# Performance work log

Measured on AMD Instinct MI355X. Metric: run time of the kernel, lower is better.

Reference implementation:

```python
import jax, jax.numpy as jnp
import numpy as np

N = 50000
E = 800000
IN_DIM = 256
HID = 256
EMB = 64


def _glorot(key, shape):
    fan_in, fan_out = shape[0], shape[1]
    lim = jnp.sqrt(6.0 / (fan_in + fan_out)).astype(jnp.float32)
    return jax.random.uniform(key, shape, jnp.float32, -lim, lim)


def sage_conv(x, src, dst, W_neigh, W_root, b, num_nodes):
    # PyG SAGEConv (aggr='mean', root_weight=True):
    #   out = mean_{j in N(i)} x_j @ W_neigh + x_i @ W_root + b
    msgs = x[src]                                              # [E, F] gather
    s = jax.ops.segment_sum(msgs, dst, num_segments=num_nodes)  # [N, F]
    cnt = jax.ops.segment_sum(jnp.ones((msgs.shape[0],), x.dtype), dst,
                              num_segments=num_nodes)           # [N]
    mean = s / jnp.maximum(cnt, 1.0)[:, None]
    return mean @ W_neigh + x @ W_root + b


def encode(x, src, dst, W1n, W1r, b1, W2n, W2r, b2):
    h = sage_conv(x, src, dst, W1n, W1r, b1, x.shape[0])
    h = jax.nn.relu(h)  # dropout omitted (eval mode)
    return sage_conv(h, src, dst, W2n, W2r, b2, x.shape[0])


def setup_inputs() -> dict:
    key = jax.random.key(0)
    ks = jax.random.split(key, 20)
    inp = {
        "user_x": jax.random.normal(ks[0], (N, IN_DIM), jnp.float32),
        "item_x": jax.random.normal(ks[1], (N, IN_DIM), jnp.float32),
        "user_edge_index": jax.random.randint(ks[2], (2, E), 0, N),
        "item_edge_index": jax.random.randint(ks[3], (2, E), 0, N),
        # user encoder params
        "u1_Wn": _glorot(ks[4], (IN_DIM, HID)), "u1_Wr": _glorot(ks[5], (IN_DIM, HID)),
        "u1_b": jnp.zeros((HID,), jnp.float32),
        "u2_Wn": _glorot(ks[6], (HID, EMB)), "u2_Wr": _glorot(ks[7], (HID, EMB)),
        "u2_b": jnp.zeros((EMB,), jnp.float32),
        # item encoder params
        "i1_Wn": _glorot(ks[8], (IN_DIM, HID)), "i1_Wr": _glorot(ks[9], (IN_DIM, HID)),
        "i1_b": jnp.zeros((HID,), jnp.float32),
        "i2_Wn": _glorot(ks[10], (HID, EMB)), "i2_Wr": _glorot(ks[11], (HID, EMB)),
        "i2_b": jnp.zeros((EMB,), jnp.float32),
        # scoring head: Linear(2*EMB, 1)
        "head_W": _glorot(ks[12], (2 * EMB, 1)),
        "head_b": jnp.zeros((1,), jnp.float32),
    }
    return inp


def reference(user_x, item_x, user_edge_index, item_edge_index,
              u1_Wn, u1_Wr, u1_b, u2_Wn, u2_Wr, u2_b,
              i1_Wn, i1_Wr, i1_b, i2_Wn, i2_Wr, i2_b,
              head_W, head_b):
    u_src, u_dst = user_edge_index[0], user_edge_index[1]
    i_src, i_dst = item_edge_index[0], item_edge_index[1]
    user_emb = encode(user_x, u_src, u_dst, u1_Wn, u1_Wr, u1_b, u2_Wn, u2_Wr, u2_b)
    item_emb = encode(item_x, i_src, i_dst, i1_Wn, i1_Wr, i1_b, i2_Wn, i2_Wr, i2_b)
    combined = jnp.concatenate([user_emb, item_emb], axis=-1)   # [N, 2*EMB]
    return jax.nn.sigmoid(combined @ head_W + head_b)           # [N, 1]
```

## Files before the change

### kernel.cpp

```cpp
#include <hip/hip_runtime.h>
#include <cstdint>
#include <cstddef>

#define N_NODES 50000
#define N_EDGES 800000
#define IN_DIM 256
#define HID 256
#define EMB 64
#define SCAN_B 1024
#define NBLK ((N_NODES + SCAN_B - 1) / SCAN_B)

typedef __attribute__((ext_vector_type(8))) short bf16x8v;
typedef __attribute__((ext_vector_type(4))) float f32x4v;

__device__ inline ushort f2bf(float f) {
    uint32_t u = __float_as_uint(f);
    uint32_t r = (u + 0x7FFFu + ((u >> 16) & 1u)) >> 16;
    return (ushort)r;
}
__device__ inline float bf2f(ushort b) {
    return __uint_as_float((uint32_t)b << 16);
}

__global__ void hist_kernel(const int* __restrict__ dst, int* __restrict__ cnt, int E) {
    int e = blockIdx.x * blockDim.x + threadIdx.x;
    if (e < E) atomicAdd(&cnt[dst[e]], 1);
}

__global__ void scan_local(const int* __restrict__ cnt, int* __restrict__ loc,
                           int* __restrict__ bsum, int n) {
    __shared__ int buf[SCAN_B];
    int tid = threadIdx.x;
    int i = blockIdx.x * SCAN_B + tid;
    int v = (i < n) ? cnt[i] : 0;
    buf[tid] = v;
    __syncthreads();
    #pragma unroll
    for (int off = 1; off < SCAN_B; off <<= 1) {
        int t = (tid >= off) ? buf[tid - off] : 0;
        __syncthreads();
        buf[tid] += t;
        __syncthreads();
    }
    if (i < n) loc[i] = buf[tid] - v;
    if (tid == SCAN_B - 1) bsum[blockIdx.x] = buf[SCAN_B - 1];
}

__global__ void scan_bsum(int* __restrict__ bsum, int nb, int* __restrict__ total_out) {
    __shared__ int b[64];
    int tid = threadIdx.x;
    int v = (tid < nb) ? bsum[tid] : 0;
    b[tid] = v;
    __syncthreads();
    #pragma unroll
    for (int off = 1; off < 64; off <<= 1) {
        int t = (tid >= off) ? b[tid - off] : 0;
        __syncthreads();
        b[tid] += t;
        __syncthreads();
    }
    if (tid < nb) bsum[tid] = b[tid] - v;
    if (tid == 63) *total_out = b[63];
}

__global__ void scan_add(int* __restrict__ loc_cursor, const int* __restrict__ bsum,
                         int* __restrict__ offs, int n) {
    int i = blockIdx.x * SCAN_B + threadIdx.x;
    if (i < n) {
        int o = loc_cursor[i] + bsum[blockIdx.x];
        offs[i] = o;
        loc_cursor[i] = o;
    }
}

__global__ void fill_kernel(const int* __restrict__ src, const int* __restrict__ dst,
                            int* __restrict__ cursor, int* __restrict__ ssrc, int E) {
    int e = blockIdx.x * blockDim.x + threadIdx.x;
    if (e < E) {
        int d = dst[e];
        int pos = atomicAdd(&cursor[d], 1);
        ssrc[pos] = src[e];
    }
}

__global__ void cvt_split(const float* __restrict__ x, ushort* __restrict__ xh,
                          ushort* __restrict__ xl, int n4) {
    int i = blockIdx.x * blockDim.x + threadIdx.x;
    if (i >= n4) return;
    float4 v = ((const float4*)x)[i];
    ushort4 h, l;
    h.x = f2bf(v.x); l.x = f2bf(v.x - bf2f(h.x));
    h.y = f2bf(v.y); l.y = f2bf(v.y - bf2f(h.y));
    h.z = f2bf(v.z); l.z = f2bf(v.z - bf2f(h.z));
    h.w = f2bf(v.w); l.w = f2bf(v.w - bf2f(h.w));
    ((ushort4*)xh)[i] = h;
    ((ushort4*)xl)[i] = l;
}

__global__ void cvt_wT(const float* __restrict__ B1, const float* __restrict__ B2,
                       ushort* __restrict__ th, ushort* __restrict__ tl, int Nhalf) {
    int idx = blockIdx.x * blockDim.x + threadIdx.x;
    if (idx >= 2 * Nhalf * 256) return;
    int nn = idx >> 8;
    int k  = idx & 255;
    const float* Bp = (nn < Nhalf) ? B1 : B2;
    int col = (nn < Nhalf) ? nn : nn - Nhalf;
    float v = Bp[(size_t)k * Nhalf + col];
    ushort h = f2bf(v);
    th[idx] = h;
    tl[idx] = f2bf(v - bf2f(h));
}

__global__ __launch_bounds__(256) void gemm_bf16x3(
        const ushort* __restrict__ Ah, const ushort* __restrict__ Al,
        const ushort* __restrict__ BTh, const ushort* __restrict__ BTl,
        ushort* __restrict__ Cb, float* __restrict__ Cf,
        int M, int nsplit, int ldf) {
    __shared__ ushort As[2][128 * 32];

    int tid  = threadIdx.x;
    int lane = tid & 63;
    int wv   = tid >> 6;
    int wm   = wv >> 1;
    int wn   = wv & 1;
    int rowBase = blockIdx.x * 128;
    int colBase = blockIdx.y * 128;

    int sr = tid & 127;
    int sm = tid >> 7;
    const ushort* Ag = sm ? Al : Ah;
    int grow = rowBase + sr;
    bool rok = grow < M;
    int sxor = (sr >> 1) & 3;

    int fr = lane & 15;
    int fc = lane >> 4;
    int axor = (fr >> 1) & 3;

    f32x4v zero4 = {0.f, 0.f, 0.f, 0.f};
    f32x4v acc[4][4];
    #pragma unroll
    for (int a = 0; a < 4; ++a)
        #pragma unroll
        for (int b = 0; b < 4; ++b) acc[a][b] = zero4;

    for (int k0 = 0; k0 < 256; k0 += 32) {
        __syncthreads();
        {
            const ushort* gs = Ag + (size_t)grow * 256 + k0;
            #pragma unroll
            for (int s = 0; s < 4; ++s) {
                uint4 v = rok ? *(const uint4*)(gs + s * 8) : make_uint4(0u, 0u, 0u, 0u);
                *(uint4*)&As[sm][sr * 32 + (s ^ sxor) * 8] = v;
            }
        }
        __syncthreads();

        bf16x8v afh[4], afl[4];
        #pragma unroll
        for (int mf = 0; mf < 4; ++mf) {
            int row = wm * 64 + mf * 16 + fr;
            int addr = row * 32 + ((fc ^ axor) * 8);
            afh[mf] = *(const bf16x8v*)&As[0][addr];
            afl[mf] = *(const bf16x8v*)&As[1][addr];
        }
        #pragma unroll
        for (int nf = 0; nf < 4; ++nf) {
            int col = colBase + wn * 64 + nf * 16 + fr;
            size_t boff = (size_t)col * 256 + k0 + fc * 8;
            bf16x8v bfh = *(const bf16x8v*)(BTh + boff);
            bf16x8v bfl = *(const bf16x8v*)(BTl + boff);
            #pragma unroll
            for (int mf = 0; mf < 4; ++mf) {
                acc[mf][nf] = __builtin_amdgcn_mfma_f32_16x16x32_bf16(
                                  afh[mf], bfh, acc[mf][nf], 0, 0, 0);
                acc[mf][nf] = __builtin_amdgcn_mfma_f32_16x16x32_bf16(
                                  afh[mf], bfl, acc[mf][nf], 0, 0, 0);
                acc[mf][nf] = __builtin_amdgcn_mfma_f32_16x16x32_bf16(
                                  afl[mf], bfh, acc[mf][nf], 0, 0, 0);
            }
        }
    }

    #pragma unroll
    for (int mf = 0; mf < 4; ++mf) {
        #pragma unroll
        for (int nf = 0; nf < 4; ++nf) {
            int col = colBase + wn * 64 + nf * 16 + fr;
            #pragma unroll
            for (int r = 0; r < 4; ++r) {
                int row = rowBase + wm * 64 + mf * 16 + fc * 4 + r;
                if (row < M) {
                    float v = acc[mf][nf][r];
                    if (col < nsplit)
                        Cb[(size_t)row * nsplit + col] = f2bf(v);
                    else
                        Cf[(size_t)row * ldf + (col - nsplit)] = v;
                }
            }
        }
    }
}

__global__ void combine1_kernel(const ushort* __restrict__ t1b,
                                const float* __restrict__ r1,
                                const int* __restrict__ offs,
                                const int* __restrict__ ssrc,
                                const float* __restrict__ b1,
                                ushort* __restrict__ hh, ushort* __restrict__ hl,
                                int n) {
    int gtid = blockIdx.x * blockDim.x + threadIdx.x;
    int node = gtid >> 6;
    int lane = gtid & 63;
    if (node >= n) return;
    int beg = offs[node];
    int end = offs[node + 1];
    const ushort4* t = (const ushort4*)t1b;
    float4 s = make_float4(0.f, 0.f, 0.f, 0.f);
    int e = beg;
    for (; e + 1 < end; e += 2) {
        int s0 = ssrc[e];
        int s1 = ssrc[e + 1];
        ushort4 q0 = t[(size_t)s0 * 64 + lane];
        ushort4 q1 = t[(size_t)s1 * 64 + lane];
        s.x += bf2f(q0.x) + bf2f(q1.x);
        s.y += bf2f(q0.y) + bf2f(q1.y);
        s.z += bf2f(q0.z) + bf2f(q1.z);
        s.w += bf2f(q0.w) + bf2f(q1.w);
    }
    if (e < end) {
        ushort4 q0 = t[(size_t)ssrc[e] * 64 + lane];
        s.x += bf2f(q0.x); s.y += bf2f(q0.y);
        s.z += bf2f(q0.z); s.w += bf2f(q0.w);
    }
    int deg = end - beg;
    float inv = 1.0f / (float)(deg > 0 ? deg : 1);
    float4 r = ((const float4*)r1)[(size_t)node * 64 + lane];
    float4 bb = ((const float4*)b1)[lane];
    float o0 = s.x * inv + r.x + bb.x;
    float o1 = s.y * inv + r.y + bb.y;
    float o2 = s.z * inv + r.z + bb.z;
    float o3 = s.w * inv + r.w + bb.w;
    o0 = o0 > 0.f ? o0 : 0.f;
    o1 = o1 > 0.f ? o1 : 0.f;
    o2 = o2 > 0.f ? o2 : 0.f;
    o3 = o3 > 0.f ? o3 : 0.f;
    ushort4 h, l;
    h.x = f2bf(o0); l.x = f2bf(o0 - bf2f(h.x));
    h.y = f2bf(o1); l.y = f2bf(o1 - bf2f(h.y));
    h.z = f2bf(o2); l.z = f2bf(o2 - bf2f(h.z));
    h.w = f2bf(o3); l.w = f2bf(o3 - bf2f(h.w));
    ((ushort4*)hh)[(size_t)node * 64 + lane] = h;
    ((ushort4*)hl)[(size_t)node * 64 + lane] = l;
}

__global__ void combine2_kernel(const ushort* __restrict__ t2b,
                                const float* __restrict__ r2,
                                const int* __restrict__ offs,
                                const int* __restrict__ ssrc,
                                const float* __restrict__ b2,
                                float* __restrict__ emb, int n) {
    int gtid = blockIdx.x * blockDim.x + threadIdx.x;
    int node = gtid >> 6;
    int lane = gtid & 63;
    if (node >= n) return;
    int beg = offs[node];
    int end = offs[node + 1];
    float s = 0.f;
    int e = beg;
    for (; e + 1 < end; e += 2) {
        int s0 = ssrc[e];
        int s1 = ssrc[e + 1];
        float v0 = bf2f(t2b[(size_t)s0 * 64 + lane]);
        float v1 = bf2f(t2b[(size_t)s1 * 64 + lane]);
        s += v0 + v1;
    }
    if (e < end) s += bf2f(t2b[(size_t)ssrc[e] * 64 + lane]);
    int deg = end - beg;
    float inv = 1.0f / (float)(deg > 0 ? deg : 1);
    emb[(size_t)node * 64 + lane] =
        s * inv + r2[(size_t)node * 64 + lane] + b2[lane];
}

__global__ void head_kernel(const float* __restrict__ eu, const float* __restrict__ ei,
                            const float* __restrict__ hW, const float* __restrict__ hb,
                            float* __restrict__ out, int n) {
    __shared__ float w[128];
    __shared__ float b0;
    if (threadIdx.x < 128) w[threadIdx.x] = hW[threadIdx.x];
    if (threadIdx.x == 0) b0 = hb[0];
    __syncthreads();
    int i = blockIdx.x * blockDim.x + threadIdx.x;
    if (i >= n) return;
    const float4* a = (const float4*)(eu + (size_t)i * 64);
    const float4* c = (const float4*)(ei + (size_t)i * 64);
    float s = b0;
    #pragma unroll
    for (int j = 0; j < 16; ++j) {
        float4 v = a[j];
        s += v.x * w[j * 4 + 0] + v.y * w[j * 4 + 1] + v.z * w[j * 4 + 2] + v.w * w[j * 4 + 3];
    }
    #pragma unroll
    for (int j = 0; j < 16; ++j) {
        float4 v = c[j];
        s += v.x * w[64 + j * 4 + 0] + v.y * w[64 + j * 4 + 1] + v.z * w[64 + j * 4 + 2] + v.w * w[64 + j * 4 + 3];
    }
    out[i] = 1.0f / (1.0f + __expf(-s));
}

extern "C" void kernel_launch(void* const* d_in, const int* in_sizes, int n_in,
                              void* d_out, int out_size, void* d_ws, size_t ws_size,
                              hipStream_t stream) {
    const float* user_x = (const float*)d_in[0];
    const float* item_x = (const float*)d_in[1];
    const int*   u_ei   = (const int*)d_in[2];
    const int*   i_ei   = (const int*)d_in[3];
    const float* u1_Wn = (const float*)d_in[4];
    const float* u1_Wr = (const float*)d_in[5];
    const float* u1_b  = (const float*)d_in[6];
    const float* u2_Wn = (const float*)d_in[7];
    const float* u2_Wr = (const float*)d_in[8];
    const float* u2_b  = (const float*)d_in[9];
    const float* i1_Wn = (const float*)d_in[10];
    const float* i1_Wr = (const float*)d_in[11];
    const float* i1_b  = (const float*)d_in[12];
    const float* i2_Wn = (const float*)d_in[13];
    const float* i2_Wr = (const float*)d_in[14];
    const float* i2_b  = (const float*)d_in[15];
    const float* head_W = (const float*)d_in[16];
    const float* head_b = (const float*)d_in[17];
    float* out = (float*)d_out;

    char* p = (char*)d_ws;
    auto alloc = [&](size_t bytes) -> void* {
        void* r = (void*)p;
        p += (bytes + 255) & ~(size_t)255;
        return r;
    };
    int* cnt_u  = (int*)alloc((size_t)N_NODES * 4);
    int* cnt_i  = (int*)alloc((size_t)N_NODES * 4);
    int* offs_u = (int*)alloc((size_t)(N_NODES + 1) * 4);
    int* offs_i = (int*)alloc((size_t)(N_NODES + 1) * 4);
    int* cur_u  = (int*)alloc((size_t)N_NODES * 4);
    int* cur_i  = (int*)alloc((size_t)N_NODES * 4);
    int* bsum_u = (int*)alloc((size_t)64 * 4);
    int* bsum_i = (int*)alloc((size_t)64 * 4);
    int* ssrc_u = (int*)alloc((size_t)N_EDGES * 4);
    int* ssrc_i = (int*)alloc((size_t)N_EDGES * 4);
    ushort* xh  = (ushort*)alloc((size_t)N_NODES * 256 * 2);
    ushort* xl  = (ushort*)alloc((size_t)N_NODES * 256 * 2);
    ushort* hh  = (ushort*)alloc((size_t)N_NODES * 256 * 2);
    ushort* hl  = (ushort*)alloc((size_t)N_NODES * 256 * 2);
    ushort* w1h = (ushort*)alloc((size_t)512 * 256 * 2);
    ushort* w1l = (ushort*)alloc((size_t)512 * 256 * 2);
    ushort* w2h = (ushort*)alloc((size_t)128 * 256 * 2);
    ushort* w2l = (ushort*)alloc((size_t)128 * 256 * 2);
    ushort* t1b = (ushort*)alloc((size_t)N_NODES * 256 * 2);
    float*  r1  = (float*)alloc((size_t)N_NODES * 256 * 4);
    ushort* t2b = (ushort*)alloc((size_t)N_NODES * 64 * 2);
    float*  r2  = (float*)alloc((size_t)N_NODES * 64 * 4);
    float* emb_u = (float*)alloc((size_t)N_NODES * EMB * 4);
    float* emb_i = (float*)alloc((size_t)N_NODES * EMB * 4);

    hipMemsetAsync(cnt_u, 0, (size_t)N_NODES * 4, stream);
    hipMemsetAsync(cnt_i, 0, (size_t)N_NODES * 4, stream);

    const int* u_src = u_ei;
    const int* u_dst = u_ei + N_EDGES;
    const int* i_src = i_ei;
    const int* i_dst = i_ei + N_EDGES;

    int egrid = (N_EDGES + 255) / 256;
    int sgrid = (N_NODES * 64 + 255) / 256;
    int mgrid128 = (N_NODES + 127) / 128;
    int cvt_x_grid = (N_NODES * 256 / 4 + 255) / 256;

    hist_kernel<<<egrid, 256, 0, stream>>>(u_dst, cnt_u, N_EDGES);
    hist_kernel<<<egrid, 256, 0, stream>>>(i_dst, cnt_i, N_EDGES);
    scan_local<<<NBLK, SCAN_B, 0, stream>>>(cnt_u, cur_u, bsum_u, N_NODES);
    scan_local<<<NBLK, SCAN_B, 0, stream>>>(cnt_i, cur_i, bsum_i, N_NODES);
    scan_bsum<<<1, 64, 0, stream>>>(bsum_u, NBLK, offs_u + N_NODES);
    scan_bsum<<<1, 64, 0, stream>>>(bsum_i, NBLK, offs_i + N_NODES);
    scan_add<<<NBLK, SCAN_B, 0, stream>>>(cur_u, bsum_u, offs_u, N_NODES);
    scan_add<<<NBLK, SCAN_B, 0, stream>>>(cur_i, bsum_i, offs_i, N_NODES);
    fill_kernel<<<egrid, 256, 0, stream>>>(u_src, u_dst, cur_u, ssrc_u, N_EDGES);
    fill_kernel<<<egrid, 256, 0, stream>>>(i_src, i_dst, cur_i, ssrc_i, N_EDGES);

    cvt_split<<<cvt_x_grid, 256, 0, stream>>>(user_x, xh, xl, N_NODES * 256 / 4);
    cvt_wT<<<(2 * 256 * 256 + 255) / 256, 256, 0, stream>>>(u1_Wn, u1_Wr, w1h, w1l, 256);
    cvt_wT<<<(2 * 64 * 256 + 255) / 256, 256, 0, stream>>>(u2_Wn, u2_Wr, w2h, w2l, 64);
    {
        dim3 g(mgrid128, 4);
        gemm_bf16x3<<<g, 256, 0, stream>>>(xh, xl, w1h, w1l, t1b, r1, N_NODES, 256, 256);
    }
    combine1_kernel<<<sgrid, 256, 0, stream>>>(t1b, r1, offs_u, ssrc_u, u1_b, hh, hl, N_NODES);
    {
        dim3 g(mgrid128, 1);
        gemm_bf16x3<<<g, 256, 0, stream>>>(hh, hl, w2h, w2l, t2b, r2, N_NODES, 64, 64);
    }
    combine2_kernel<<<sgrid, 256, 0, stream>>>(t2b, r2, offs_u, ssrc_u, u2_b, emb_u, N_NODES);

    cvt_split<<<cvt_x_grid, 256, 0, stream>>>(item_x, xh, xl, N_NODES * 256 / 4);
    cvt_wT<<<(2 * 256 * 256 + 255) / 256, 256, 0, stream>>>(i1_Wn, i1_Wr, w1h, w1l, 256);
    cvt_wT<<<(2 * 64 * 256 + 255) / 256, 256, 0, stream>>>(i2_Wn, i2_Wr, w2h, w2l, 64);
    {
        dim3 g(mgrid128, 4);
        gemm_bf16x3<<<g, 256, 0, stream>>>(xh, xl, w1h, w1l, t1b, r1, N_NODES, 256, 256);
    }
    combine1_kernel<<<sgrid, 256, 0, stream>>>(t1b, r1, offs_i, ssrc_i, i1_b, hh, hl, N_NODES);
    {
        dim3 g(mgrid128, 1);
        gemm_bf16x3<<<g, 256, 0, stream>>>(hh, hl, w2h, w2l, t2b, r2, N_NODES, 64, 64);
    }
    combine2_kernel<<<sgrid, 256, 0, stream>>>(t2b, r2, offs_i, ssrc_i, i2_b, emb_i, N_NODES);

    head_kernel<<<(N_NODES + 255) / 256, 256, 0, stream>>>(emb_u, emb_i, head_W,
                                                           head_b, out, N_NODES);
}
```

Baseline: 892.6 us.

## Stage full-K A row panel in LDS once and loop over column groups

The GEMM now loads a 64-row by 256-K panel of both hi and lo A operands into shared memory once per block, then iterates over column groups of 128 inside the block. Previously each block reloaded A per 128-column tile, with a K-loop and two barriers per step. This cuts redundant A reads from global memory and removes the per-K synchronisation. The cost is 64KB of LDS per block, which lowers occupancy, and each block now does up to four column groups serially.

```diff
diff --git a/kernel.cpp b/kernel.cpp
--- a/kernel.cpp
+++ b/kernel.cpp
@@ -9,6 +9,7 @@
 #define EMB 64
 #define SCAN_B 1024
 #define NBLK ((N_NODES + SCAN_B - 1) / SCAN_B)
+#define BR 64
 
 typedef __attribute__((ext_vector_type(8))) short bf16x8v;
 typedef __attribute__((ext_vector_type(4))) float f32x4v;
@@ -111,91 +112,90 @@
     tl[idx] = f2bf(v - bf2f(h));
 }
 
-__global__ __launch_bounds__(256) void gemm_bf16x3(
+__global__ __launch_bounds__(256) void gemm_bf16x3_v2(
         const ushort* __restrict__ Ah, const ushort* __restrict__ Al,
         const ushort* __restrict__ BTh, const ushort* __restrict__ BTl,
         ushort* __restrict__ Cb, float* __restrict__ Cf,
-        int M, int nsplit, int ldf) {
-    __shared__ ushort As[2][128 * 32];
+        int M, int nsplit, int ldf, int ncg) {
+    __shared__ ushort As[2][BR * 256];
 
     int tid  = threadIdx.x;
     int lane = tid & 63;
     int wv   = tid >> 6;
     int wm   = wv >> 1;
     int wn   = wv & 1;
-    int rowBase = blockIdx.x * 128;
-    int colBase = blockIdx.y * 128;
-
-    int sr = tid & 127;
-    int sm = tid >> 7;
-    const ushort* Ag = sm ? Al : Ah;
-    int grow = rowBase + sr;
-    bool rok = grow < M;
-    int sxor = (sr >> 1) & 3;
+    int rowBase = blockIdx.x * BR;
+
+    #pragma unroll
+    for (int i = 0; i < 16; ++i) {
+        int gidx = i * 256 + tid;
+        int sm   = gidx >> 11;
+        int rem  = gidx & 2047;
+        int row  = rem >> 5;
+        int slot = rem & 31;
+        const ushort* Ag = sm ? Al : Ah;
+        int gr = rowBase + row;
+        uint4 v = (gr < M) ? *(const uint4*)(Ag + (size_t)gr * 256 + slot * 8)
+                           : make_uint4(0u, 0u, 0u, 0u);
+        *(uint4*)&As[sm][row * 256 + ((slot ^ (row & 7)) * 8)] = v;
+    }
+    __syncthreads();
 
     int fr = lane & 15;
     int fc = lane >> 4;
-    int axor = (fr >> 1) & 3;
-
-    f32x4v zero4 = {0.f, 0.f, 0.f, 0.f};
-    f32x4v acc[4][4];
-    #pragma unroll
-    for (int a = 0; a < 4; ++a)
+
+    for (int cg = 0; cg < ncg; ++cg) {
+        f32x4v zero4 = {0.f, 0.f, 0.f, 0.f};
+        f32x4v acc[2][4];
         #pragma unroll
-        for (int b = 0; b < 4; ++b) acc[a][b] = zero4;
-
-    for (int k0 = 0; k0 < 256; k0 += 32) {
-        __syncthreads();
-        {
-            const ushort* gs = Ag + (size_t)grow * 256 + k0;
+        for (int a = 0; a < 2; ++a)
             #pragma unroll
-            for (int s = 0; s < 4; ++s) {
-                uint4 v = rok ? *(const uint4*)(gs + s * 8) : make_uint4(0u, 0u, 0u, 0u);
-                *(uint4*)&As[sm][sr * 32 + (s ^ sxor) * 8] = v;
+            for (int b = 0; b < 4; ++b) acc[a][b] = zero4;
+
+        #pragma unroll
+        for (int k0 = 0; k0 < 8; ++k0) {
+            bf16x8v afh[2], afl[2];
+            #pragma unroll
+            for (int mf = 0; mf < 2; ++mf) {
+                int row   = wm * 32 + mf * 16 + fr;
+                int kslot = (k0 * 4 + fc) ^ (row & 7);
+                int addr  = row * 256 + kslot * 8;
+                afh[mf] = *(const bf16x8v*)&As[0][addr];
+                afl[mf] = *(const bf16x8v*)&As[1][addr];
+            }
+            #pragma unroll
+            for (int nf = 0; nf < 4; ++nf) {
+                int col = cg * 128 + wn * 64 + nf * 16 + fr;
+                size_t boff = (size_t)col * 256 + k0 * 32 + fc * 8;
+                bf16x8v bfh = *(const bf16x8v*)(BTh + boff);
+                bf16x8v bfl = *(const bf16x8v*)(BTl + boff);
+                #pragma unroll
+                for (int mf = 0; mf < 2; ++mf) {
+                    acc[mf][nf] = __builtin_amdgcn_mfma_f32_16x16x32_bf16(
+                                      afh[mf], bfh, acc[mf][nf], 0, 0, 0);
+                    acc[mf][nf] = __builtin_amdgcn_mfma_f32_16x16x32_bf16(
+                                      afh[mf], bfl, acc[mf][nf], 0, 0, 0);
+                    acc[mf][nf] = __builtin_amdgcn_mfma_f32_16x16x32_bf16(
+                                      afl[mf], bfh, acc[mf][nf], 0, 0, 0);
+                }
             }
         }
-        __syncthreads();
-
-        bf16x8v afh[4], afl[4];
+
         #pragma unroll
-        for (int mf = 0; mf < 4; ++mf) {
-            int row = wm * 64 + mf * 16 + fr;
-            int addr = row * 32 + ((fc ^ axor) * 8);
-            afh[mf] = *(const bf16x8v*)&As[0][addr];
-            afl[mf] = *(const bf16x8v*)&As[1][addr];
-        }
-        #pragma unroll
-        for (int nf = 0; nf < 4; ++nf) {
-            int col = colBase + wn * 64 + nf * 16 + fr;
-            size_t boff = (size_t)col * 256 + k0 + fc * 8;
-            bf16x8v bfh = *(const bf16x8v*)(BTh + boff);
-            bf16x8v bfl = *(const bf16x8v*)(BTl + boff);
+        for (int mf = 0; mf < 2; ++mf) {
             #pragma unroll
-            for (int mf = 0; mf < 4; ++mf) {
-                acc[mf][nf] = __builtin_amdgcn_mfma_f32_16x16x32_bf16(
-                                  afh[mf], bfh, acc[mf][nf], 0, 0, 0);
-                acc[mf][nf] = __builtin_amdgcn_mfma_f32_16x16x32_bf16(
-                                  afh[mf], bfl, acc[mf][nf], 0, 0, 0);
-                acc[mf][nf] = __builtin_amdgcn_mfma_f32_16x16x32_bf16(
-                                  afl[mf], bfh, acc[mf][nf], 0, 0, 0);
-            }
-        }
-    }
-
-    #pragma unroll
-    for (int mf = 0; mf < 4; ++mf) {
-        #pragma unroll
-        for (int nf = 0; nf < 4; ++nf) {
-            int col = colBase + wn * 64 + nf * 16 + fr;
-            #pragma unroll
-            for (int r = 0; r < 4; ++r) {
-                int row = rowBase + wm * 64 + mf * 16 + fc * 4 + r;
-                if (row < M) {
-                    float v = acc[mf][nf][r];
-                    if (col < nsplit)
-                        Cb[(size_t)row * nsplit + col] = f2bf(v);
-                    else
-                        Cf[(size_t)row * ldf + (col - nsplit)] = v;
+            for (int nf = 0; nf < 4; ++nf) {
+                int col = cg * 128 + wn * 64 + nf * 16 + fr;
+                #pragma unroll
+                for (int r = 0; r < 4; ++r) {
+                    int row = rowBase + wm * 32 + mf * 16 + fc * 4 + r;
+                    if (row < M) {
+                        float v = acc[mf][nf][r];
+                        if (col < nsplit)
+                            Cb[(size_t)row * nsplit + col] = f2bf(v);
+                        else
+                            Cf[(size_t)row * ldf + (col - nsplit)] = v;
+                    }
                 }
             }
         }
@@ -372,7 +372,7 @@
 
     int egrid = (N_EDGES + 255) / 256;
     int sgrid = (N_NODES * 64 + 255) / 256;
-    int mgrid128 = (N_NODES + 127) / 128;
+    int mgrid64 = (N_NODES + BR - 1) / BR;
     int cvt_x_grid = (N_NODES * 256 / 4 + 255) / 256;
 
     hist_kernel<<<egrid, 256, 0, stream>>>(u_dst, cnt_u, N_EDGES);
@@ -389,29 +389,21 @@
     cvt_split<<<cvt_x_grid, 256, 0, stream>>>(user_x, xh, xl, N_NODES * 256 / 4);
     cvt_wT<<<(2 * 256 * 256 + 255) / 256, 256, 0, stream>>>(u1_Wn, u1_Wr, w1h, w1l, 256);
     cvt_wT<<<(2 * 64 * 256 + 255) / 256, 256, 0, stream>>>(u2_Wn, u2_Wr, w2h, w2l, 64);
-    {
-        dim3 g(mgrid128, 4);
-        gemm_bf16x3<<<g, 256, 0, stream>>>(xh, xl, w1h, w1l, t1b, r1, N_NODES, 256, 256);
-    }
+    gemm_bf16x3_v2<<<mgrid64, 256, 0, stream>>>(xh, xl, w1h, w1l, t1b, r1,
+                                                N_NODES, 256, 256, 4);
     combine1_kernel<<<sgrid, 256, 0, stream>>>(t1b, r1, offs_u, ssrc_u, u1_b, hh, hl, N_NODES);
-    {
-        dim3 g(mgrid128, 1);
-        gemm_bf16x3<<<g, 256, 0, stream>>>(hh, hl, w2h, w2l, t2b, r2, N_NODES, 64, 64);
-    }
+    gemm_bf16x3_v2<<<mgrid64, 256, 0, stream>>>(hh, hl, w2h, w2l, t2b, r2,
+                                                N_NODES, 64, 64, 1);
     combine2_kernel<<<sgrid, 256, 0, stream>>>(t2b, r2, offs_u, ssrc_u, u2_b, emb_u, N_NODES);
 
     cvt_split<<<cvt_x_grid, 256, 0, stream>>>(item_x, xh, xl, N_NODES * 256 / 4);
     cvt_wT<<<(2 * 256 * 256 + 255) / 256, 256, 0, stream>>>(i1_Wn, i1_Wr, w1h, w1l, 256);
     cvt_wT<<<(2 * 64 * 256 + 255) / 256, 256, 0, stream>>>(i2_Wn, i2_Wr, w2h, w2l, 64);
-    {
-        dim3 g(mgrid128, 4);
-        gemm_bf16x3<<<g, 256, 0, stream>>>(xh, xl, w1h, w1l, t1b, r1, N_NODES, 256, 256);
-    }
+    gemm_bf16x3_v2<<<mgrid64, 256, 0, stream>>>(xh, xl, w1h, w1l, t1b, r1,
+                                                N_NODES, 256, 256, 4);
     combine1_kernel<<<sgrid, 256, 0, stream>>>(t1b, r1, offs_i, ssrc_i, i1_b, hh, hl, N_NODES);
-    {
-        dim3 g(mgrid128, 1);
-        gemm_bf16x3<<<g, 256, 0, stream>>>(hh, hl, w2h, w2l, t2b, r2, N_NODES, 64, 64);
-    }
+    gemm_bf16x3_v2<<<mgrid64, 256, 0, stream>>>(hh, hl, w2h, w2l, t2b, r2,
+                                                N_NODES, 64, 64, 1);
     combine2_kernel<<<sgrid, 256, 0, stream>>>(t2b, r2, offs_i, ssrc_i, i2_b, emb_i, N_NODES);
 
     head_kernel<<<(N_NODES + 255) / 256, 256, 0, stream>>>(emb_u, emb_i, head_W,
```

Result: slower. 984.9 us (+10.3%).

## Double-buffer A tile in LDS with register prefetch in bf16x3 GEMM

Applied to the files above, without the earlier changes.

The bf16x3 GEMM now prefetches the next 32-wide K slice of A into registers while running MFMAs on the current slice. It then writes that slice into a second LDS buffer, so each K step needs one barrier instead of two. The global load pattern is also reorganised so four consecutive threads cover one 64-byte row segment across 32 rows. This doubles LDS use and raises register pressure, which may lower occupancy.

```diff
diff --git a/kernel.cpp b/kernel.cpp
--- a/kernel.cpp
+++ b/kernel.cpp
@@ -111,12 +111,12 @@
     tl[idx] = f2bf(v - bf2f(h));
 }
 
-__global__ __launch_bounds__(256) void gemm_bf16x3(
+__global__ __launch_bounds__(256) void gemm_bf16x3_v3(
         const ushort* __restrict__ Ah, const ushort* __restrict__ Al,
         const ushort* __restrict__ BTh, const ushort* __restrict__ BTl,
         ushort* __restrict__ Cb, float* __restrict__ Cf,
         int M, int nsplit, int ldf) {
-    __shared__ ushort As[2][128 * 32];
+    __shared__ ushort As[2][2][128 * 32];
 
     int tid  = threadIdx.x;
     int lane = tid & 63;
@@ -126,12 +126,31 @@
     int rowBase = blockIdx.x * 128;
     int colBase = blockIdx.y * 128;
 
-    int sr = tid & 127;
-    int sm = tid >> 7;
+    int sm   = tid >> 7;
+    int t    = tid & 127;
+    int slot = t & 3;
+    int r0   = t >> 2;
     const ushort* Ag = sm ? Al : Ah;
-    int grow = rowBase + sr;
-    bool rok = grow < M;
-    int sxor = (sr >> 1) & 3;
+
+    uint4 st[4];
+    auto issue = [&](int k0) {
+        #pragma unroll
+        for (int j = 0; j < 4; ++j) {
+            int row = r0 + j * 32;
+            int gr  = rowBase + row;
+            st[j] = (gr < M)
+                  ? *(const uint4*)(Ag + (size_t)gr * 256 + k0 * 32 + slot * 8)
+                  : make_uint4(0u, 0u, 0u, 0u);
+        }
+    };
+    auto stwrite = [&](int buf) {
+        #pragma unroll
+        for (int j = 0; j < 4; ++j) {
+            int row = r0 + j * 32;
+            int sx  = (row >> 1) & 3;
+            *(uint4*)&As[buf][sm][row * 32 + ((slot ^ sx) * 8)] = st[j];
+        }
+    };
 
     int fr = lane & 15;
     int fc = lane >> 4;
@@ -144,30 +163,26 @@
         #pragma unroll
         for (int b = 0; b < 4; ++b) acc[a][b] = zero4;
 
-    for (int k0 = 0; k0 < 256; k0 += 32) {
-        __syncthreads();
-        {
-            const ushort* gs = Ag + (size_t)grow * 256 + k0;
-            #pragma unroll
-            for (int s = 0; s < 4; ++s) {
-                uint4 v = rok ? *(const uint4*)(gs + s * 8) : make_uint4(0u, 0u, 0u, 0u);
-                *(uint4*)&As[sm][sr * 32 + (s ^ sxor) * 8] = v;
-            }
-        }
-        __syncthreads();
+    issue(0);
+    stwrite(0);
+    __syncthreads();
+
+    for (int k0 = 0; k0 < 8; ++k0) {
+        int cur = k0 & 1;
+        if (k0 < 7) issue(k0 + 1);
 
         bf16x8v afh[4], afl[4];
         #pragma unroll
         for (int mf = 0; mf < 4; ++mf) {
-            int row = wm * 64 + mf * 16 + fr;
+            int row  = wm * 64 + mf * 16 + fr;
             int addr = row * 32 + ((fc ^ axor) * 8);
-            afh[mf] = *(const bf16x8v*)&As[0][addr];
-            afl[mf] = *(const bf16x8v*)&As[1][addr];
+            afh[mf] = *(const bf16x8v*)&As[cur][0][addr];
+            afl[mf] = *(const bf16x8v*)&As[cur][1][addr];
         }
         #pragma unroll
         for (int nf = 0; nf < 4; ++nf) {
             int col = colBase + wn * 64 + nf * 16 + fr;
-            size_t boff = (size_t)col * 256 + k0 + fc * 8;
+            size_t boff = (size_t)col * 256 + k0 * 32 + fc * 8;
             bf16x8v bfh = *(const bf16x8v*)(BTh + boff);
             bf16x8v bfl = *(const bf16x8v*)(BTl + boff);
             #pragma unroll
@@ -180,6 +195,9 @@
                                   afl[mf], bfh, acc[mf][nf], 0, 0, 0);
             }
         }
+
+        if (k0 < 7) stwrite((k0 + 1) & 1);
+        __syncthreads();
     }
 
     #pragma unroll
@@ -391,12 +409,12 @@
     cvt_wT<<<(2 * 64 * 256 + 255) / 256, 256, 0, stream>>>(u2_Wn, u2_Wr, w2h, w2l, 64);
     {
         dim3 g(mgrid128, 4);
-        gemm_bf16x3<<<g, 256, 0, stream>>>(xh, xl, w1h, w1l, t1b, r1, N_NODES, 256, 256);
+        gemm_bf16x3_v3<<<g, 256, 0, stream>>>(xh, xl, w1h, w1l, t1b, r1, N_NODES, 256, 256);
     }
     combine1_kernel<<<sgrid, 256, 0, stream>>>(t1b, r1, offs_u, ssrc_u, u1_b, hh, hl, N_NODES);
     {
         dim3 g(mgrid128, 1);
-        gemm_bf16x3<<<g, 256, 0, stream>>>(hh, hl, w2h, w2l, t2b, r2, N_NODES, 64, 64);
+        gemm_bf16x3_v3<<<g, 256, 0, stream>>>(hh, hl, w2h, w2l, t2b, r2, N_NODES, 64, 64);
     }
     combine2_kernel<<<sgrid, 256, 0, stream>>>(t2b, r2, offs_u, ssrc_u, u2_b, emb_u, N_NODES);
 
@@ -405,12 +423,12 @@
     cvt_wT<<<(2 * 64 * 256 + 255) / 256, 256, 0, stream>>>(i2_Wn, i2_Wr, w2h, w2l, 64);
     {
         dim3 g(mgrid128, 4);
-        gemm_bf16x3<<<g, 256, 0, stream>>>(xh, xl, w1h, w1l, t1b, r1, N_NODES, 256, 256);
+        gemm_bf16x3_v3<<<g, 256, 0, stream>>>(xh, xl, w1h, w1l, t1b, r1, N_NODES, 256, 256);
     }
     combine1_kernel<<<sgrid, 256, 0, stream>>>(t1b, r1, offs_i, ssrc_i, i1_b, hh, hl, N_NODES);
     {
         dim3 g(mgrid128, 1);
-        gemm_bf16x3<<<g, 256, 0, stream>>>(hh, hl, w2h, w2l, t2b, r2, N_NODES, 64, 64);
+        gemm_bf16x3_v3<<<g, 256, 0, stream>>>(hh, hl, w2h, w2l, t2b, r2, N_NODES, 64, 64);
     }
     combine2_kernel<<<sgrid, 256, 0, stream>>>(t2b, r2, offs_i, ssrc_i, i2_b, emb_i, N_NODES);
 
```

Result: faster. 866.8 us (-2.9%).
